# Performance work log

Measured on AMD Instinct MI355X. Metric: run time of the kernel, lower is better.

Reference implementation:

```python
import jax, jax.numpy as jnp
import numpy as np

EPS = 1e-5

def conv1x1(x, w, b):
    # x: (B,C,H,W), w: (O,C), b: (O,)
    return jnp.einsum('bchw,oc->bohw', x, w) + b[None, :, None, None]

def instance_norm(x):
    mu = jnp.mean(x, axis=(2, 3), keepdims=True)
    var = jnp.var(x, axis=(2, 3), keepdims=True)
    return (x - mu) / jnp.sqrt(var + EPS)

def setup_inputs() -> dict:
    key = jax.random.key(0)
    C = 256
    ks = jax.random.split(key, 16)
    def w(k):
        return jax.random.normal(k, (C, C), dtype=jnp.float32) * 0.02
    def b(k):
        return jax.random.normal(k, (C,), dtype=jnp.float32) * 0.01
    return {
        'x': jax.random.normal(ks[0], (8, C, 128, 128), dtype=jnp.float32),
        'wq1': w(ks[1]), 'bq1': b(ks[2]), 'wq2': w(ks[3]), 'bq2': b(ks[4]),
        'wk1': w(ks[5]), 'bk1': b(ks[6]), 'wk2': w(ks[7]), 'bk2': b(ks[8]),
        'wv': w(ks[9]), 'bv': b(ks[10]),
        'wg': w(ks[11]), 'bg': b(ks[12]),
        'wo': w(ks[13]), 'bo': b(ks[14]),
    }

def reference(x, wq1, bq1, wq2, bq2, wk1, bk1, wk2, bk2, wv, bv, wg, bg, wo, bo):
    head = 4
    B, C, H, W = x.shape
    c = C // head  # per-head channels
    n = H * W
    x = instance_norm(x)
    q = jax.nn.softplus(conv1x1(jax.nn.gelu(conv1x1(x, wq1, bq1), approximate=False), wq2, bq2))
    k = jax.nn.softplus(conv1x1(jax.nn.gelu(conv1x1(x, wk1, bk1), approximate=False), wk2, bk2))
    v = jax.nn.gelu(conv1x1(x, wv, bv), approximate=False)
    g = jax.nn.gelu(conv1x1(x, wg, bg), approximate=False)
    # b (head c) h w -> b head c (h w)
    q = q.reshape(B, head, c, n)
    kk = k.reshape(B, head, c, n)
    vv = v.reshape(B, head, c, n)
    kv = jnp.einsum('bhcn,bhdn->bhcd', kk, vv)  # (B,head,c,c)
    scale = 1.0 / jnp.sqrt(jnp.float32(c))
    z = jnp.einsum('bhcn,bhc->bhn', q, kk.sum(axis=-1)) * scale
    z = 1.0 / (z + jnp.float32(n))
    out = jnp.einsum('bhcn,bhcd->bhdn', q, kv) * scale
    out = (out + vv) * z[:, :, None, :]
    out = out.reshape(B, C, H, W)
    out = out * g
    return conv1x1(out, wo, bo)
```

## Files before the change

### kernel.cpp

```cpp
#include <hip/hip_runtime.h>
#include <stdint.h>

typedef short bf8 __attribute__((ext_vector_type(8)));
typedef short s4v __attribute__((ext_vector_type(4)));
typedef float f32x4 __attribute__((ext_vector_type(4)));

__device__ __forceinline__ short f2bf(float f){
  union { float f; unsigned u; } c; c.f = f;
  unsigned r = (c.u + 0x7fffu + ((c.u >> 16) & 1u)) >> 16;
  return (short)r;
}
__device__ __forceinline__ float bf2f(short s){
  union { unsigned u; float f; } c; c.u = ((unsigned)(unsigned short)s) << 16;
  return c.f;
}
__device__ __forceinline__ void gload16(const void* g, void* l){
  __builtin_amdgcn_global_load_lds((const __attribute__((address_space(1))) uint32_t*)g,
                                   (__attribute__((address_space(3))) uint32_t*)l, 16, 0, 0);
}
__device__ __forceinline__ float fast_erf(float x){
  const float s = fabsf(x);
  const float t = __builtin_amdgcn_rcpf(fmaf(0.3275911f, s, 1.0f));
  float p = fmaf(1.061405429f, t, -1.453152027f);
  p = fmaf(p, t, 1.421413741f);
  p = fmaf(p, t, -0.284496736f);
  p = fmaf(p, t, 0.254829592f);
  p = p * t;
  const float e = __expf(-s * s);
  return copysignf(fmaf(-p, e, 1.0f), x);
}
__device__ __forceinline__ float act_gelu(float x){
  return 0.5f * x * (1.0f + fast_erf(x * 0.70710678118654752f));
}
__device__ __forceinline__ float act_softplus(float x){
  const float e = __expf(-fabsf(x));
  return fmaxf(x, 0.0f) + __logf(1.0f + e);
}

__global__ __launch_bounds__(256) void k_stats(const float* __restrict__ x,
                                               float* __restrict__ mu, float* __restrict__ rsig){
  const int row = blockIdx.x;
  const float4* xr = (const float4*)(x + (size_t)row * 16384);
  float s1 = 0.f, s2 = 0.f;
  for (int i = threadIdx.x; i < 4096; i += 256){
    float4 v = xr[i];
    s1 += v.x + v.y + v.z + v.w;
    s2 += v.x*v.x + v.y*v.y + v.z*v.z + v.w*v.w;
  }
  __shared__ float a1[256], a2[256];
  a1[threadIdx.x] = s1; a2[threadIdx.x] = s2; __syncthreads();
  for (int s = 128; s > 0; s >>= 1){
    if (threadIdx.x < s){ a1[threadIdx.x] += a1[threadIdx.x+s]; a2[threadIdx.x] += a2[threadIdx.x+s]; }
    __syncthreads();
  }
  if (threadIdx.x == 0){
    float m = a1[0] * (1.0f/16384.0f);
    float v = a2[0] * (1.0f/16384.0f) - m*m;
    mu[row] = m; rsig[row] = rsqrtf(v + 1e-5f);
  }
}

__global__ __launch_bounds__(256) void k_normt(const float* __restrict__ x, const float* __restrict__ mu,
                                               const float* __restrict__ rsig, short* __restrict__ xn){
  const int n0 = blockIdx.x * 64, c0 = blockIdx.y * 64, b = blockIdx.z;
  __shared__ short lt[64][68];
  const int t = threadIdx.x;
  const int nj = (t & 15) * 4, cb = t >> 4;
#pragma unroll
  for (int it = 0; it < 4; ++it){
    const int ci = cb + it * 16;
    const int row = b * 256 + c0 + ci;
    const float m = mu[row], rs = rsig[row];
    float4 v = *(const float4*)(x + (size_t)row * 16384 + n0 + nj);
    s4v o;
    o[0] = f2bf((v.x - m) * rs); o[1] = f2bf((v.y - m) * rs);
    o[2] = f2bf((v.z - m) * rs); o[3] = f2bf((v.w - m) * rs);
    *(s4v*)(&lt[ci][nj]) = o;
  }
  __syncthreads();
#pragma unroll
  for (int p = 0; p < 2; ++p){
    const int q = p * 256 + t;
    const int nl = q >> 3, c8 = (q & 7) * 8;
    bf8 o;
#pragma unroll
    for (int j = 0; j < 8; ++j) o[j] = lt[c8 + j][nl];
    *(bf8*)(xn + ((size_t)(b * 16384 + n0 + nl)) * 256 + c0 + c8) = o;
  }
}

__global__ __launch_bounds__(256) void k_wconv(const float* w0, const float* w1, const float* w2,
                                               const float* w3, const float* w4, const float* w5,
                                               const float* w6, short* __restrict__ wb){
  const int gid = blockIdx.x * 256 + threadIdx.x;
  const int mat = gid >> 14, r4 = gid & 16383;
  const float* srcs[7] = {w0, w1, w2, w3, w4, w5, w6};
  float4 v = *(const float4*)(srcs[mat] + (size_t)r4 * 4);
  s4v o; o[0] = f2bf(v.x); o[1] = f2bf(v.y); o[2] = f2bf(v.z); o[3] = f2bf(v.w);
  *(s4v*)(wb + (size_t)mat * 65536 + r4 * 4) = o;
}

template<int ACT, int OUTMODE>
__global__ __launch_bounds__(256, 2)
void k_gemm(const short* __restrict__ A, const short* __restrict__ W,
            const float* __restrict__ bias, void* __restrict__ outv){
  __shared__ short sm[12288];
  short* sA = sm;
  short* sB = sm + 4096;
  const int t = threadIdx.x, l = t & 63, w = t >> 6;
  const int wr = w >> 1, wc = w & 1;
  const int lm = l & 15, lk = l >> 4;
  const size_t m0 = (size_t)blockIdx.x * 128;
  const int swz = ((lk ^ ((lm >> 1) & 3)) << 4);
  f32x4 acc[4][8] = {};

  for (int ks = 0; ks < 8; ++ks){
    const int k0 = ks * 32;
#pragma unroll
    for (int p = 0; p < 2; ++p){
      const int q = p * 256 + t, r = q >> 2, kc = q & 3;
      gload16(A + (m0 + r) * 256 + k0 + ((kc ^ ((r >> 1) & 3)) << 3),
              (char*)sA + (p * 256 + w * 64) * 16);
    }
#pragma unroll
    for (int p = 0; p < 4; ++p){
      const int q = p * 256 + t, r = q >> 2, kc = q & 3;
      gload16(W + (size_t)r * 256 + k0 + ((kc ^ ((r >> 1) & 3)) << 3),
              (char*)sB + (p * 256 + w * 64) * 16);
    }
    __syncthreads();
    bf8 af[4], bfv[8];
#pragma unroll
    for (int mi = 0; mi < 4; ++mi)
      af[mi] = *(const bf8*)((const char*)sA + (wr * 64 + mi * 16 + lm) * 64 + swz);
#pragma unroll
    for (int ni = 0; ni < 8; ++ni)
      bfv[ni] = *(const bf8*)((const char*)sB + (wc * 128 + ni * 16 + lm) * 64 + swz);
#pragma unroll
    for (int mi = 0; mi < 4; ++mi)
#pragma unroll
      for (int ni = 0; ni < 8; ++ni)
        acc[mi][ni] = __builtin_amdgcn_mfma_f32_16x16x32_bf16(af[mi], bfv[ni], acc[mi][ni], 0, 0, 0);
    __syncthreads();
  }

  if constexpr (OUTMODE == 0){
    __shared__ short rp[32 * 264];
    short* outp = (short*)outv;
#pragma unroll
    for (int mi = 0; mi < 4; ++mi){
      __syncthreads();
      const int rloc = wr * 16 + lk * 4;
#pragma unroll
      for (int ni = 0; ni < 8; ++ni){
        const int o = wc * 128 + ni * 16 + lm;
        const float bi = bias[o];
#pragma unroll
        for (int j = 0; j < 4; ++j){
          float v = acc[mi][ni][j] + bi;
          if (ACT == 1) v = act_gelu(v);
          else if (ACT == 2) v = act_softplus(v);
          rp[(rloc + j) * 264 + o] = f2bf(v);
        }
      }
      __syncthreads();
#pragma unroll
      for (int it = 0; it < 4; ++it){
        const int q = it * 256 + t, rr = q >> 5, c = q & 31;
        const int gr = (rr >> 4) * 64 + mi * 16 + (rr & 15);
        *(bf8*)(outp + (m0 + gr) * 256 + c * 8) = *(const bf8*)(rp + rr * 264 + c * 8);
      }
    }
  } else {
    float* outp = (float*)outv;
    const size_t b = m0 >> 14;
    const int nb = (int)(m0 & 16383);
#pragma unroll
    for (int mi = 0; mi < 4; ++mi){
      const int np = nb + wr * 64 + mi * 16 + lk * 4;
#pragma unroll
      for (int ni = 0; ni < 8; ++ni){
        const int o = wc * 128 + ni * 16 + lm;
        const float bi = bias[o];
        float4 v;
        v.x = acc[mi][ni][0] + bi; v.y = acc[mi][ni][1] + bi;
        v.z = acc[mi][ni][2] + bi; v.w = acc[mi][ni][3] + bi;
        *(float4*)(outp + ((b * 256 + o) * 16384 + np)) = v;
      }
    }
  }
}

__global__ __launch_bounds__(256, 2)
void k_chain(const short* __restrict__ A, const short* __restrict__ W1, const float* __restrict__ b1,
             const short* __restrict__ W2, const float* __restrict__ b2, short* __restrict__ out){
  __shared__ short sA[64 * 32];
  __shared__ short sB[256 * 32];
  __shared__ short h1[64 * 256];
  const int t = threadIdx.x, l = t & 63, w = t >> 6;
  const int lm = l & 15, lk = l >> 4;
  const size_t m0 = (size_t)blockIdx.x * 64;
  const int swz = ((lk ^ ((lm >> 1) & 3)) << 4);
  f32x4 acc[4][4] = {};

  for (int ks = 0; ks < 8; ++ks){
    const int k0 = ks * 32;
    {
      const int r = t >> 2, kc = t & 3;
      gload16(A + (m0 + r) * 256 + k0 + ((kc ^ ((r >> 1) & 3)) << 3),
              (char*)sA + w * 1024);
    }
#pragma unroll
    for (int p = 0; p < 4; ++p){
      const int q = p * 256 + t, r = q >> 2, kc = q & 3;
      gload16(W1 + (size_t)r * 256 + k0 + ((kc ^ ((r >> 1) & 3)) << 3),
              (char*)sB + (p * 256 + w * 64) * 16);
    }
    __syncthreads();
    bf8 af[4], bfv[4];
#pragma unroll
    for (int mi = 0; mi < 4; ++mi)
      af[mi] = *(const bf8*)((const char*)sA + (mi * 16 + lm) * 64 + swz);
#pragma unroll
    for (int ni = 0; ni < 4; ++ni)
      bfv[ni] = *(const bf8*)((const char*)sB + (w * 64 + ni * 16 + lm) * 64 + swz);
#pragma unroll
    for (int mi = 0; mi < 4; ++mi)
#pragma unroll
      for (int ni = 0; ni < 4; ++ni)
        acc[mi][ni] = __builtin_amdgcn_mfma_f32_16x16x32_bf16(af[mi], bfv[ni], acc[mi][ni], 0, 0, 0);
    __syncthreads();
  }
#pragma unroll
  for (int mi = 0; mi < 4; ++mi)
#pragma unroll
    for (int ni = 0; ni < 4; ++ni){
      const int col = w * 64 + ni * 16 + lm;
      const float bi = b1[col];
#pragma unroll
      for (int j = 0; j < 4; ++j){
        const int row = mi * 16 + lk * 4 + j;
        const float v = act_gelu(acc[mi][ni][j] + bi);
        const int byte = row * 512 + ((((col >> 3) ^ (row & 7)) << 4) | ((col & 7) << 1));
        *(short*)((char*)h1 + byte) = f2bf(v);
      }
      acc[mi][ni] = (f32x4){0.f, 0.f, 0.f, 0.f};
    }
  __syncthreads();

  for (int ks = 0; ks < 8; ++ks){
    const int k0 = ks * 32;
#pragma unroll
    for (int p = 0; p < 4; ++p){
      const int q = p * 256 + t, r = q >> 2, kc = q & 3;
      gload16(W2 + (size_t)r * 256 + k0 + ((kc ^ ((r >> 1) & 3)) << 3),
              (char*)sB + (p * 256 + w * 64) * 16);
    }
    __syncthreads();
    bf8 af[4], bfv[4];
#pragma unroll
    for (int mi = 0; mi < 4; ++mi){
      const int row = mi * 16 + lm;
      const int slot = (ks * 4 + lk) ^ (row & 7);
      af[mi] = *(const bf8*)((const char*)h1 + row * 512 + (slot << 4));
    }
#pragma unroll
    for (int ni = 0; ni < 4; ++ni)
      bfv[ni] = *(const bf8*)((const char*)sB + (w * 64 + ni * 16 + lm) * 64 + swz);
#pragma unroll
    for (int mi = 0; mi < 4; ++mi)
#pragma unroll
      for (int ni = 0; ni < 4; ++ni)
        acc[mi][ni] = __builtin_amdgcn_mfma_f32_16x16x32_bf16(af[mi], bfv[ni], acc[mi][ni], 0, 0, 0);
    __syncthreads();
  }
#pragma unroll
  for (int mi = 0; mi < 4; ++mi)
#pragma unroll
    for (int ni = 0; ni < 4; ++ni){
      const int col = w * 64 + ni * 16 + lm;
      const float bi = b2[col];
#pragma unroll
      for (int j = 0; j < 4; ++j){
        const int row = mi * 16 + lk * 4 + j;
        const float v = act_softplus(acc[mi][ni][j] + bi);
        const int byte = row * 512 + ((((col >> 3) ^ (row & 7)) << 4) | ((col & 7) << 1));
        *(short*)((char*)h1 + byte) = f2bf(v);
      }
    }
  __syncthreads();
#pragma unroll
  for (int it = 0; it < 8; ++it){
    const int idx = it * 256 + t, r = idx >> 5, s = idx & 31;
    *(bf8*)(out + (m0 + r) * 256 + s * 8) =
        *(const bf8*)((const char*)h1 + r * 512 + (((s ^ (r & 7)) << 4)));
  }
}

__global__ __launch_bounds__(256) void k_kv(const short* __restrict__ kg, const short* __restrict__ vg,
                                            float* __restrict__ kvpart, float* __restrict__ kspart){
  const int s = blockIdx.x, h = blockIdx.y, b = blockIdx.z;
  __shared__ short sk[64 * 72], sv[64 * 72];
  __shared__ float pl[256][8];
  const int t = threadIdx.x, l = t & 63, w = t >> 6;
  const int lm = l & 15, lk = l >> 4;
  float ksp[8];
#pragma unroll
  for (int j = 0; j < 8; ++j) ksp[j] = 0.f;
  f32x4 acc[4] = {};
  const size_t rowbase = ((size_t)b * 16384 + s * 2048) * 256 + h * 64;

  for (int tt = 0; tt < 32; ++tt){
    __syncthreads();
#pragma unroll
    for (int p = 0; p < 2; ++p){
      const int q = p * 256 + t;
      const int nl = q >> 3, c8 = (q & 7) * 8;
      bf8 kvv = *(const bf8*)(kg + rowbase + (size_t)(tt * 64 + nl) * 256 + c8);
      bf8 vvv = *(const bf8*)(vg + rowbase + (size_t)(tt * 64 + nl) * 256 + c8);
#pragma unroll
      for (int j = 0; j < 8; ++j){
        sk[(c8 + j) * 72 + nl] = kvv[j];
        sv[(c8 + j) * 72 + nl] = vvv[j];
        ksp[j] += bf2f(kvv[j]);
      }
    }
    __syncthreads();
#pragma unroll
    for (int ks = 0; ks < 2; ++ks){
      bf8 ak = *(const bf8*)((const char*)sk + (w * 16 + lm) * 144 + ks * 64 + lk * 16);
#pragma unroll
      for (int ni = 0; ni < 4; ++ni){
        bf8 bv = *(const bf8*)((const char*)sv + (ni * 16 + lm) * 144 + ks * 64 + lk * 16);
        acc[ni] = __builtin_amdgcn_mfma_f32_16x16x32_bf16(ak, bv, acc[ni], 0, 0, 0);
      }
    }
  }
#pragma unroll
  for (int j = 0; j < 8; ++j) pl[t][j] = ksp[j];
  __syncthreads();
  const size_t slot = (size_t)(b * 4 + h) * 8 + s;
  if (t < 64){
    float sum = 0.f;
    const int g8 = t >> 3, j = t & 7;
    for (int m = 0; m < 32; ++m) sum += pl[m * 8 + g8][j];
    kspart[slot * 64 + t] = sum;
  }
  float* kvp = kvpart + slot * 4096;
#pragma unroll
  for (int ni = 0; ni < 4; ++ni)
#pragma unroll
    for (int j = 0; j < 4; ++j){
      const int c = w * 16 + lk * 4 + j, d = ni * 16 + lm;
      kvp[c * 64 + d] = acc[ni][j];
    }
}

__global__ __launch_bounds__(256) void k_kvred(const float* __restrict__ kvpart, const float* __restrict__ kspart,
                                               short* __restrict__ kvT, float* __restrict__ ksum_s){
  const int gid = blockIdx.x * 256 + threadIdx.x;
#pragma unroll
  for (int i = 0; i < 8; ++i){
    const int o = gid * 8 + i;
    const int bh = o >> 12, rem = o & 4095, d = rem >> 6, c = rem & 63;
    float sum = 0.f;
#pragma unroll
    for (int s = 0; s < 8; ++s) sum += kvpart[((size_t)bh * 8 + s) * 4096 + c * 64 + d];
    kvT[o] = f2bf(sum * 0.125f);
  }
  if (gid < 2048){
    float sum = 0.f;
#pragma unroll
    for (int s = 0; s < 8; ++s) sum += kspart[((size_t)(gid >> 6) * 8 + s) * 64 + (gid & 63)];
    ksum_s[gid] = sum * 0.125f;
  }
}

__global__ __launch_bounds__(256, 2) void k_attn(const short* __restrict__ qg, const short* __restrict__ vg,
                                                 const short* __restrict__ gg, const short* __restrict__ kvT,
                                                 const float* __restrict__ ksum_s, short* __restrict__ y){
  const int n0 = blockIdx.x * 64, b = blockIdx.y;
  __shared__ short sq[64 * 264];
  __shared__ short skv[256 * 72];
  __shared__ float sz[256];
  __shared__ float sks[256];
  const int t = threadIdx.x, l = t & 63, w = t >> 6;
  const int lm = l & 15, lk = l >> 4;
  const size_t mrow = (size_t)b * 16384 + n0;

#pragma unroll
  for (int it = 0; it < 8; ++it){
    const int q = it * 256 + t, p = q >> 5, c16 = (q & 31) * 8;
    *(bf8*)((char*)sq + p * 528 + c16 * 2) = *(const bf8*)(qg + (mrow + p) * 256 + c16);
  }
  const short* kvb = kvT + (size_t)b * 16384;
#pragma unroll
  for (int it = 0; it < 8; ++it){
    const int q = it * 256 + t, r = q >> 3, c8 = (q & 7) * 8;
    *(bf8*)((char*)skv + r * 144 + c8 * 2) = *(const bf8*)(kvb + r * 64 + c8);
  }
  sks[t] = ksum_s[b * 256 + t];
  __syncthreads();

  {
    const int p = t & 63, h = t >> 6;
    float dot = 0.f;
#pragma unroll
    for (int cc = 0; cc < 8; ++cc){
      bf8 qv = *(const bf8*)((const char*)sq + p * 528 + (h * 64 + cc * 8) * 2);
#pragma unroll
      for (int j = 0; j < 8; ++j) dot += bf2f(qv[j]) * sks[h * 64 + cc * 8 + j];
    }
    sz[h * 64 + p] = 1.0f / (dot + 16384.0f);
  }

  const int h = w;
  f32x4 acc[4][4] = {};
#pragma unroll
  for (int ks = 0; ks < 2; ++ks){
    bf8 aq[4];
#pragma unroll
    for (int mi = 0; mi < 4; ++mi)
      aq[mi] = *(const bf8*)((const char*)sq + (mi * 16 + lm) * 528 + h * 128 + ks * 64 + lk * 16);
#pragma unroll
    for (int ni = 0; ni < 4; ++ni){
      bf8 bk = *(const bf8*)((const char*)skv + (h * 64 + ni * 16 + lm) * 144 + ks * 64 + lk * 16);
#pragma unroll
      for (int mi = 0; mi < 4; ++mi)
        acc[mi][ni] = __builtin_amdgcn_mfma_f32_16x16x32_bf16(aq[mi], bk, acc[mi][ni], 0, 0, 0);
    }
  }
#pragma unroll
  for (int mi = 0; mi < 4; ++mi)
#pragma unroll
    for (int ni = 0; ni < 4; ++ni){
      const int d = ni * 16 + lm, ch = h * 64 + d;
#pragma unroll
      for (int j = 0; j < 4; ++j){
        const int p = mi * 16 + lk * 4 + j;
        const float vf = bf2f(vg[(mrow + p) * 256 + ch]);
        const float gf = bf2f(gg[(mrow + p) * 256 + ch]);
        const float o = (acc[mi][ni][j] + vf) * sz[h * 64 + p] * gf;
        sq[p * 264 + ch] = f2bf(o);
      }
    }
  __syncthreads();
#pragma unroll
  for (int it = 0; it < 8; ++it){
    const int q = it * 256 + t, p = q >> 5, c16 = (q & 31) * 8;
    *(bf8*)(y + (mrow + p) * 256 + c16) = *(const bf8*)((const char*)sq + p * 528 + c16 * 2);
  }
}

extern "C" void kernel_launch(void* const* d_in, const int* in_sizes, int n_in,
                              void* d_out, int out_size, void* d_ws, size_t ws_size,
                              hipStream_t stream){
  (void)in_sizes; (void)n_in; (void)out_size; (void)ws_size;
  const float* x   = (const float*)d_in[0];
  const float* wq1 = (const float*)d_in[1];
  const float* bq1 = (const float*)d_in[2];
  const float* wq2 = (const float*)d_in[3];
  const float* bq2 = (const float*)d_in[4];
  const float* wk1 = (const float*)d_in[5];
  const float* bk1 = (const float*)d_in[6];
  const float* wk2 = (const float*)d_in[7];
  const float* bk2 = (const float*)d_in[8];
  const float* wv  = (const float*)d_in[9];
  const float* bv  = (const float*)d_in[10];
  const float* wg  = (const float*)d_in[11];
  const float* bg  = (const float*)d_in[12];
  const float* wo  = (const float*)d_in[13];
  const float* bo  = (const float*)d_in[14];

  char* ws = (char*)d_ws;
  float* mu     = (float*)(ws + 0);
  float* rsig   = (float*)(ws + 8192);
  short* wb     = (short*)(ws + 16384);
  float* kvpart = (float*)(ws + 933888);
  float* kspart = (float*)(ws + 5128192);
  short* kvT    = (short*)(ws + 5193728);
  float* ksum_s = (float*)(ws + 5455872);
  short* B0 = (short*)(ws + 8388608);
  short* B1 = B0 + 33554432;
  short* B2 = B1 + 33554432;
  short* B3 = B2 + 33554432;

  k_wconv<<<448, 256, 0, stream>>>(wq1, wq2, wk1, wk2, wv, wg, wo, wb);
  k_stats<<<2048, 256, 0, stream>>>(x, mu, rsig);
  k_normt<<<dim3(256, 4, 8), 256, 0, stream>>>(x, mu, rsig, B0);
  k_chain<<<2048, 256, 0, stream>>>(B0, wb + 0 * 65536, bq1, wb + 1 * 65536, bq2, B2);
  k_chain<<<2048, 256, 0, stream>>>(B0, wb + 2 * 65536, bk1, wb + 3 * 65536, bk2, B3);
  k_gemm<1, 0><<<1024, 256, 0, stream>>>(B0, wb + 4 * 65536, bv, B1);
  k_kv<<<dim3(8, 4, 8), 256, 0, stream>>>(B3, B1, kvpart, kspart);
  k_kvred<<<64, 256, 0, stream>>>(kvpart, kspart, kvT, ksum_s);
  k_gemm<1, 0><<<1024, 256, 0, stream>>>(B0, wb + 5 * 65536, bg, B3);
  k_attn<<<dim3(256, 8), 256, 0, stream>>>(B2, B1, B3, kvT, ksum_s, B0);
  k_gemm<0, 1><<<1024, 256, 0, stream>>>(B0, wb + 6 * 65536, bo, d_out);
}
```

Baseline: 467.9 us.

## Swap MFMA operands to write transposed accumulators directly and drop LDS staging

Swaps the A/B operands of the MFMA calls in the pixel-major GEMM, fused MLP and attention kernels, so each lane holds four consecutive output channels for one pixel. The epilogues then write 8-byte vectors straight to global memory (or to the swizzled LDS hidden buffer) instead of staging through a shared-memory tile with extra barriers. The attention kernel also stops staging q in LDS and reads it directly from global, and raises launch bounds to 3 blocks per SM because less LDS is used. The trade is narrower, less coalesced global stores and redundant global q reads in exchange for fewer barriers, less LDS traffic and higher occupancy.

```diff
diff --git a/kernel.cpp b/kernel.cpp
--- a/kernel.cpp
+++ b/kernel.cpp
@@ -139,36 +139,33 @@
 #pragma unroll
     for (int mi = 0; mi < 4; ++mi)
 #pragma unroll
-      for (int ni = 0; ni < 8; ++ni)
-        acc[mi][ni] = __builtin_amdgcn_mfma_f32_16x16x32_bf16(af[mi], bfv[ni], acc[mi][ni], 0, 0, 0);
+      for (int ni = 0; ni < 8; ++ni){
+        if constexpr (OUTMODE == 0)
+          acc[mi][ni] = __builtin_amdgcn_mfma_f32_16x16x32_bf16(bfv[ni], af[mi], acc[mi][ni], 0, 0, 0);
+        else
+          acc[mi][ni] = __builtin_amdgcn_mfma_f32_16x16x32_bf16(af[mi], bfv[ni], acc[mi][ni], 0, 0, 0);
+      }
     __syncthreads();
   }
 
   if constexpr (OUTMODE == 0){
-    __shared__ short rp[32 * 264];
     short* outp = (short*)outv;
 #pragma unroll
-    for (int mi = 0; mi < 4; ++mi){
-      __syncthreads();
-      const int rloc = wr * 16 + lk * 4;
-#pragma unroll
-      for (int ni = 0; ni < 8; ++ni){
-        const int o = wc * 128 + ni * 16 + lm;
-        const float bi = bias[o];
+    for (int ni = 0; ni < 8; ++ni){
+      const int ob = wc * 128 + ni * 16 + lk * 4;
+      const float4 b4 = *(const float4*)(bias + ob);
+#pragma unroll
+      for (int mi = 0; mi < 4; ++mi){
+        const int px = wr * 64 + mi * 16 + lm;
+        s4v o4;
 #pragma unroll
         for (int j = 0; j < 4; ++j){
-          float v = acc[mi][ni][j] + bi;
+          float v = acc[mi][ni][j] + ((const float*)&b4)[j];
           if (ACT == 1) v = act_gelu(v);
           else if (ACT == 2) v = act_softplus(v);
-          rp[(rloc + j) * 264 + o] = f2bf(v);
+          o4[j] = f2bf(v);
         }
-      }
-      __syncthreads();
-#pragma unroll
-      for (int it = 0; it < 4; ++it){
-        const int q = it * 256 + t, rr = q >> 5, c = q & 31;
-        const int gr = (rr >> 4) * 64 + mi * 16 + (rr & 15);
-        *(bf8*)(outp + (m0 + gr) * 256 + c * 8) = *(const bf8*)(rp + rr * 264 + c * 8);
+        *(s4v*)(outp + (m0 + px) * 256 + ob) = o4;
       }
     }
   } else {
@@ -228,24 +225,25 @@
     for (int mi = 0; mi < 4; ++mi)
 #pragma unroll
       for (int ni = 0; ni < 4; ++ni)
-        acc[mi][ni] = __builtin_amdgcn_mfma_f32_16x16x32_bf16(af[mi], bfv[ni], acc[mi][ni], 0, 0, 0);
-    __syncthreads();
-  }
-#pragma unroll
-  for (int mi = 0; mi < 4; ++mi)
-#pragma unroll
-    for (int ni = 0; ni < 4; ++ni){
-      const int col = w * 64 + ni * 16 + lm;
-      const float bi = b1[col];
-#pragma unroll
-      for (int j = 0; j < 4; ++j){
-        const int row = mi * 16 + lk * 4 + j;
-        const float v = act_gelu(acc[mi][ni][j] + bi);
-        const int byte = row * 512 + ((((col >> 3) ^ (row & 7)) << 4) | ((col & 7) << 1));
-        *(short*)((char*)h1 + byte) = f2bf(v);
-      }
+        acc[mi][ni] = __builtin_amdgcn_mfma_f32_16x16x32_bf16(bfv[ni], af[mi], acc[mi][ni], 0, 0, 0);
+    __syncthreads();
+  }
+#pragma unroll
+  for (int ni = 0; ni < 4; ++ni){
+    const int ob = w * 64 + ni * 16 + lk * 4;
+    const float4 b4 = *(const float4*)(b1 + ob);
+#pragma unroll
+    for (int mi = 0; mi < 4; ++mi){
+      const int px = mi * 16 + lm;
+      s4v o4;
+#pragma unroll
+      for (int j = 0; j < 4; ++j)
+        o4[j] = f2bf(act_gelu(acc[mi][ni][j] + ((const float*)&b4)[j]));
+      const int slot = (ob >> 3) ^ (px & 7);
+      *(s4v*)((char*)h1 + px * 512 + (slot << 4) + (ob & 4) * 2) = o4;
       acc[mi][ni] = (f32x4){0.f, 0.f, 0.f, 0.f};
     }
+  }
   __syncthreads();
 
   for (int ks = 0; ks < 8; ++ks){
@@ -271,29 +269,22 @@
     for (int mi = 0; mi < 4; ++mi)
 #pragma unroll
       for (int ni = 0; ni < 4; ++ni)
-        acc[mi][ni] = __builtin_amdgcn_mfma_f32_16x16x32_bf16(af[mi], bfv[ni], acc[mi][ni], 0, 0, 0);
-    __syncthreads();
-  }
-#pragma unroll
-  for (int mi = 0; mi < 4; ++mi)
-#pragma unroll
-    for (int ni = 0; ni < 4; ++ni){
-      const int col = w * 64 + ni * 16 + lm;
-      const float bi = b2[col];
-#pragma unroll
-      for (int j = 0; j < 4; ++j){
-        const int row = mi * 16 + lk * 4 + j;
-        const float v = act_softplus(acc[mi][ni][j] + bi);
-        const int byte = row * 512 + ((((col >> 3) ^ (row & 7)) << 4) | ((col & 7) << 1));
-        *(short*)((char*)h1 + byte) = f2bf(v);
-      }
-    }
-  __syncthreads();
-#pragma unroll
-  for (int it = 0; it < 8; ++it){
-    const int idx = it * 256 + t, r = idx >> 5, s = idx & 31;
-    *(bf8*)(out + (m0 + r) * 256 + s * 8) =
-        *(const bf8*)((const char*)h1 + r * 512 + (((s ^ (r & 7)) << 4)));
+        acc[mi][ni] = __builtin_amdgcn_mfma_f32_16x16x32_bf16(bfv[ni], af[mi], acc[mi][ni], 0, 0, 0);
+    __syncthreads();
+  }
+#pragma unroll
+  for (int ni = 0; ni < 4; ++ni){
+    const int ob = w * 64 + ni * 16 + lk * 4;
+    const float4 b4 = *(const float4*)(b2 + ob);
+#pragma unroll
+    for (int mi = 0; mi < 4; ++mi){
+      const int px = mi * 16 + lm;
+      s4v o4;
+#pragma unroll
+      for (int j = 0; j < 4; ++j)
+        o4[j] = f2bf(act_softplus(acc[mi][ni][j] + ((const float*)&b4)[j]));
+      *(s4v*)(out + (m0 + px) * 256 + ob) = o4;
+    }
   }
 }
 
@@ -376,23 +367,18 @@
   }
 }
 
-__global__ __launch_bounds__(256, 2) void k_attn(const short* __restrict__ qg, const short* __restrict__ vg,
+__global__ __launch_bounds__(256, 3) void k_attn(const short* __restrict__ qg, const short* __restrict__ vg,
                                                  const short* __restrict__ gg, const short* __restrict__ kvT,
                                                  const float* __restrict__ ksum_s, short* __restrict__ y){
   const int n0 = blockIdx.x * 64, b = blockIdx.y;
-  __shared__ short sq[64 * 264];
   __shared__ short skv[256 * 72];
   __shared__ float sz[256];
   __shared__ float sks[256];
   const int t = threadIdx.x, l = t & 63, w = t >> 6;
   const int lm = l & 15, lk = l >> 4;
   const size_t mrow = (size_t)b * 16384 + n0;
-
-#pragma unroll
-  for (int it = 0; it < 8; ++it){
-    const int q = it * 256 + t, p = q >> 5, c16 = (q & 31) * 8;
-    *(bf8*)((char*)sq + p * 528 + c16 * 2) = *(const bf8*)(qg + (mrow + p) * 256 + c16);
-  }
+  const int h = w;
+
   const short* kvb = kvT + (size_t)b * 16384;
 #pragma unroll
   for (int it = 0; it < 8; ++it){
@@ -403,52 +389,48 @@
   __syncthreads();
 
   {
-    const int p = t & 63, h = t >> 6;
+    const int p = l;
     float dot = 0.f;
 #pragma unroll
     for (int cc = 0; cc < 8; ++cc){
-      bf8 qv = *(const bf8*)((const char*)sq + p * 528 + (h * 64 + cc * 8) * 2);
+      bf8 qv = *(const bf8*)(qg + (mrow + p) * 256 + h * 64 + cc * 8);
 #pragma unroll
       for (int j = 0; j < 8; ++j) dot += bf2f(qv[j]) * sks[h * 64 + cc * 8 + j];
     }
     sz[h * 64 + p] = 1.0f / (dot + 16384.0f);
   }
 
-  const int h = w;
   f32x4 acc[4][4] = {};
 #pragma unroll
   for (int ks = 0; ks < 2; ++ks){
     bf8 aq[4];
 #pragma unroll
     for (int mi = 0; mi < 4; ++mi)
-      aq[mi] = *(const bf8*)((const char*)sq + (mi * 16 + lm) * 528 + h * 128 + ks * 64 + lk * 16);
+      aq[mi] = *(const bf8*)(qg + (mrow + mi * 16 + lm) * 256 + h * 64 + ks * 32 + lk * 8);
 #pragma unroll
     for (int ni = 0; ni < 4; ++ni){
       bf8 bk = *(const bf8*)((const char*)skv + (h * 64 + ni * 16 + lm) * 144 + ks * 64 + lk * 16);
 #pragma unroll
       for (int mi = 0; mi < 4; ++mi)
-        acc[mi][ni] = __builtin_amdgcn_mfma_f32_16x16x32_bf16(aq[mi], bk, acc[mi][ni], 0, 0, 0);
-    }
-  }
-#pragma unroll
-  for (int mi = 0; mi < 4; ++mi)
+        acc[mi][ni] = __builtin_amdgcn_mfma_f32_16x16x32_bf16(bk, aq[mi], acc[mi][ni], 0, 0, 0);
+    }
+  }
+#pragma unroll
+  for (int mi = 0; mi < 4; ++mi){
+    const int px = mi * 16 + lm;
+    const float zf = sz[h * 64 + px];
+    const size_t base = (mrow + px) * 256;
 #pragma unroll
     for (int ni = 0; ni < 4; ++ni){
-      const int d = ni * 16 + lm, ch = h * 64 + d;
-#pragma unroll
-      for (int j = 0; j < 4; ++j){
-        const int p = mi * 16 + lk * 4 + j;
-        const float vf = bf2f(vg[(mrow + p) * 256 + ch]);
-        const float gf = bf2f(gg[(mrow + p) * 256 + ch]);
-        const float o = (acc[mi][ni][j] + vf) * sz[h * 64 + p] * gf;
-        sq[p * 264 + ch] = f2bf(o);
-      }
-    }
-  __syncthreads();
-#pragma unroll
-  for (int it = 0; it < 8; ++it){
-    const int q = it * 256 + t, p = q >> 5, c16 = (q & 31) * 8;
-    *(bf8*)(y + (mrow + p) * 256 + c16) = *(const bf8*)((const char*)sq + p * 528 + c16 * 2);
+      const int ch = h * 64 + ni * 16 + lk * 4;
+      s4v v4 = *(const s4v*)(vg + base + ch);
+      s4v g4 = *(const s4v*)(gg + base + ch);
+      s4v o4;
+#pragma unroll
+      for (int j = 0; j < 4; ++j)
+        o4[j] = f2bf((acc[mi][ni][j] + bf2f(v4[j])) * zf * bf2f(g4[j]));
+      *(s4v*)(y + base + ch) = o4;
+    }
   }
 }
 
```

Result: slower. 494.4 us (+5.7%).
